# Performance work log

Measured on AMD Instinct MI355X. Metric: run time of the kernel, lower is better.

## Reference

```python
import jax, jax.numpy as jnp
import numpy as np

DECAY = 0.99
COMMIT = 0.25
EPS = 1e-5


def setup_inputs() -> dict:
    key = jax.random.key(0)
    k1, k2, k3 = jax.random.split(key, 3)
    B, H, W, D, K = 32, 32, 32, 64, 1024
    return {
        "z": jax.random.normal(k1, (B, H, W, D), dtype=jnp.float32),
        "embeddings": jax.random.normal(k2, (K, D), dtype=jnp.float32),
        "cluster_size": jnp.ones((K,), dtype=jnp.float32),
        "ema_embed": jax.random.normal(k3, (K, D), dtype=jnp.float32),
    }


def reference(z, embeddings, cluster_size, ema_embed):
    B, H, W, D = z.shape
    K = embeddings.shape[0]
    z_flat = z.reshape(-1, D)                      # [N, D]

    # squared L2 distances via expansion: ||z||^2 + ||e||^2 - 2 z e^T  -> [N, K]
    distances = (
        jnp.sum(z_flat * z_flat, axis=1, keepdims=True)
        + jnp.sum(embeddings * embeddings, axis=1)
        - 2.0 * z_flat @ embeddings.T
    )
    idx = jnp.argmin(distances, axis=1)            # [N]
    quantized = embeddings[idx].reshape(z.shape)   # gather, [B,H,W,D]

    # training-mode EMA update (one_hot^T matmuls expressed as segment sums)
    n_i = jax.ops.segment_sum(jnp.ones(z_flat.shape[0], z.dtype), idx, num_segments=K)
    dw = jax.ops.segment_sum(z_flat, idx, num_segments=K)          # [K, D]
    new_cluster = cluster_size * DECAY + n_i * (1.0 - DECAY)
    new_ema = ema_embed * DECAY + dw * (1.0 - DECAY)
    n = jnp.sum(new_cluster)
    new_cluster = (new_cluster + EPS) / (n + K * EPS) * n           # Laplace smoothing
    new_embeddings = new_ema / new_cluster[:, None]

    loss = COMMIT * jnp.mean((z - jax.lax.stop_gradient(quantized)) ** 2)
    q_ste = z + jax.lax.stop_gradient(quantized - z)                # straight-through

    quantized_vectors = jnp.transpose(q_ste, (0, 3, 1, 2))          # [B, D, H, W]
    quantized_indices = idx.reshape(B, H, W)[:, None, :, :]         # [B, 1, H, W]
    return quantized_vectors, quantized_indices, loss, new_embeddings, new_cluster, new_ema
```

## Files before the change

kernel.cpp:

```cpp
#include <hip/hip_runtime.h>


typedef unsigned short u16;
typedef u16 us8 __attribute__((ext_vector_type(8)));
typedef float f4 __attribute__((ext_vector_type(4)));

#define WS_FZ    0
#define WS_FE    1
#define WS_FCS   2
#define WS_FEMA  3
#define WS_LOSS  4

__device__ __forceinline__ float b2f(u16 u) {
    union { unsigned int i; float f; } x; x.i = ((unsigned int)u) << 16; return x.f;
}
__device__ __forceinline__ int swzE(int d, int c) {
    return d * 64 + (c ^ ((((d) >> 2) & 7) << 2));
}
__device__ __forceinline__ int swzZ(int d, int c) {
    int cb = (c >> 2) ^ (c >> 5);
    int cc = ((cb & 31) << 2) | (c & 3);
    return d * 128 + (cc ^ ((((d) >> 2) & 7) << 2));
}

__global__ __launch_bounds__(256) void k_init(
    const u16* z, const u16* e, const u16* cs, const u16* ema,
    float* __restrict__ ws, float* __restrict__ esqp, int K)
{
    __shared__ int flg[4];
    const int w = threadIdx.x >> 6, l = threadIdx.x & 63;
    const u16* p = (w == 0) ? z : (w == 1) ? e : (w == 2) ? cs : ema;
    int cnt = 0;
    #pragma unroll
    for (int t = 0; t < 4; ++t) {
        unsigned hb = (p[(l * 4 + t) * 2] >> 8) & 0x7F;
        cnt += (hb >= 0x3A && hb <= 0x41) ? 1 : 0;
    }
    #pragma unroll
    for (int off = 32; off; off >>= 1) cnt += __shfl_down(cnt, off);
    if (l == 0) flg[w] = (cnt < 128) ? 1 : 0;
    __syncthreads();
    if (blockIdx.x == 0) {
        if (threadIdx.x < 4) ((int*)ws)[threadIdx.x] = flg[threadIdx.x];
        if (threadIdx.x == 4) ws[WS_LOSS] = 0.0f;
    }
    const int fe = flg[1];
    const int code = blockIdx.x * 256 + threadIdx.x;
    if (code < K) {
        float r[8];
        if (fe) {
            const float* ep = (const float*)e + (size_t)code * 64;
            #pragma unroll
            for (int j = 0; j < 8; ++j) { float v = ep[j]; float p2 = v * v;
                asm volatile("" : "+v"(p2)); r[j] = p2; }
            #pragma unroll
            for (int t = 1; t < 8; ++t)
                #pragma unroll
                for (int j = 0; j < 8; ++j) { float v = ep[8 * t + j]; float p2 = v * v;
                    asm volatile("" : "+v"(p2)); r[j] += p2; }
        } else {
            const u16* ep = e + (size_t)code * 64;
            #pragma unroll
            for (int j = 0; j < 8; ++j) { float v = b2f(ep[j]); float p2 = v * v;
                asm volatile("" : "+v"(p2)); r[j] = p2; }
            #pragma unroll
            for (int t = 1; t < 8; ++t)
                #pragma unroll
                for (int j = 0; j < 8; ++j) { float v = b2f(ep[8 * t + j]); float p2 = v * v;
                    asm volatile("" : "+v"(p2)); r[j] += p2; }
        }
        esqp[code] = ((r[0] + r[1]) + (r[2] + r[3])) + ((r[4] + r[5]) + (r[6] + r[7]));
    }
}

__global__ __launch_bounds__(512, 2) void k_main(
    const u16* __restrict__ z, const u16* __restrict__ e,
    const float* __restrict__ esqp,
    float* __restrict__ ws, float* __restrict__ out,
    int K, int offIdx, long long outSize)
{
    __shared__ __align__(16) float z_t[64 * 128];
    __shared__ __align__(16) float e_t[4 * 64 * 64];
    __shared__ float esq_l[2048];
    __shared__ float z2_l[128];
    __shared__ int   idx_l[128];

    const int tid = threadIdx.x;
    const int cg  = tid >> 7;
    const int lt  = tid & 127;
    const int mtg = lt & 15;
    const int ktg = lt >> 4;
    const int pbase = blockIdx.x * 128;
    const int* wsi = (const int*)ws;
    const int fz = wsi[WS_FZ];
    const int fe = wsi[WS_FE];
    const int kchunks = K >> 6;
    const int h = kchunks >> 2;

    for (int i = tid; i < K; i += 512) esq_l[i] = esqp[i];

    if (fz) {
        const f4* z4 = (const f4*)((const float*)z + (size_t)pbase * 64);
        for (int i = tid; i < 2048; i += 512) {
            f4 v = z4[i];
            int m = i >> 4, d4 = (i & 15) * 4;
            z_t[swzZ(d4 + 0, m)] = v[0];
            z_t[swzZ(d4 + 1, m)] = v[1];
            z_t[swzZ(d4 + 2, m)] = v[2];
            z_t[swzZ(d4 + 3, m)] = v[3];
        }
    } else {
        const us8* z8 = (const us8*)(z + (size_t)pbase * 64);
        for (int i = tid; i < 1024; i += 512) {
            us8 v = z8[i];
            int m = i >> 3, d8 = (i & 7) * 8;
            #pragma unroll
            for (int t = 0; t < 8; ++t) z_t[swzZ(d8 + t, m)] = b2f(v[t]);
        }
    }
    __syncthreads();
    if (tid < 128) {
        float r[8];
        #pragma unroll
        for (int j = 0; j < 8; ++j) {
            float v = z_t[swzZ(j, tid)]; float p = v * v;
            asm volatile("" : "+v"(p)); r[j] = p;
        }
        #pragma unroll
        for (int t = 1; t < 8; ++t)
            #pragma unroll
            for (int j = 0; j < 8; ++j) {
                float v = z_t[swzZ(8 * t + j, tid)]; float p = v * v;
                asm volatile("" : "+v"(p)); r[j] += p;
            }
        z2_l[tid] = ((r[0] + r[1]) + (r[2] + r[3])) + ((r[4] + r[5]) + (r[6] + r[7]));
    }

    float bestd[8] = {INFINITY, INFINITY, INFINITY, INFINITY,
                      INFINITY, INFINITY, INFINITY, INFINITY};
    int   besti[8] = {0, 0, 0, 0, 0, 0, 0, 0};
    float* et = e_t + cg * 4096;

    f4  fb[8];
    us8 hb[4];
    {
        int kc0 = cg * h;
        if (fe) {
            const f4* e4 = (const f4*)((const float*)e + (size_t)kc0 * 4096);
            #pragma unroll
            for (int t = 0; t < 8; ++t) fb[t] = e4[lt + 128 * t];
        } else {
            const us8* e8 = (const us8*)(e + (size_t)kc0 * 4096);
            #pragma unroll
            for (int t = 0; t < 4; ++t) hb[t] = e8[lt + 128 * t];
        }
    }

    for (int c = 0; c < h; ++c) {
        const int kc = cg * h + c;
        if (fe) {
            #pragma unroll
            for (int t = 0; t < 8; ++t) {
                int i = lt + 128 * t;
                int kl = i >> 4, d4 = (i & 15) * 4;
                et[swzE(d4 + 0, kl)] = fb[t][0];
                et[swzE(d4 + 1, kl)] = fb[t][1];
                et[swzE(d4 + 2, kl)] = fb[t][2];
                et[swzE(d4 + 3, kl)] = fb[t][3];
            }
        } else {
            #pragma unroll
            for (int t = 0; t < 4; ++t) {
                int i = lt + 128 * t;
                int kl = i >> 3, d8 = (i & 7) * 8;
                #pragma unroll
                for (int s = 0; s < 8; ++s) et[swzE(d8 + s, kl)] = b2f(hb[t][s]);
            }
        }
        if (c + 1 < h) {
            if (fe) {
                const f4* e4 = (const f4*)((const float*)e + (size_t)(kc + 1) * 4096);
                #pragma unroll
                for (int t = 0; t < 8; ++t) fb[t] = e4[lt + 128 * t];
            } else {
                const us8* e8 = (const us8*)(e + (size_t)(kc + 1) * 4096);
                #pragma unroll
                for (int t = 0; t < 4; ++t) hb[t] = e8[lt + 128 * t];
            }
        }
        __syncthreads();

        float acc[8][8] = {};
        for (int d0 = 0; d0 < 64; d0 += 4) {
            f4 za[4], zb[4], ea[4], eb[4];
            #pragma unroll
            for (int j = 0; j < 4; ++j) {
                int d = d0 + j;
                za[j] = *(const f4*)&z_t[swzZ(d, mtg * 8)];
                zb[j] = *(const f4*)&z_t[swzZ(d, mtg * 8 + 4)];
                ea[j] = *(const f4*)&et[swzE(d, ktg * 8)];
                eb[j] = *(const f4*)&et[swzE(d, ktg * 8 + 4)];
            }
            #pragma unroll
            for (int j = 0; j < 4; ++j) {
                #pragma unroll
                for (int a = 0; a < 4; ++a)
                    #pragma unroll
                    for (int b = 0; b < 4; ++b) {
                        acc[a][b]         += za[j][a] * ea[j][b];
                        acc[a][b + 4]     += za[j][a] * eb[j][b];
                        acc[a + 4][b]     += zb[j][a] * ea[j][b];
                        acc[a + 4][b + 4] += zb[j][a] * eb[j][b];
                    }
            }
        }
        __syncthreads();

        #pragma unroll
        for (int a = 0; a < 8; ++a) {
            float z2 = z2_l[mtg * 8 + a];
            #pragma unroll
            for (int b = 0; b < 8; ++b) {
                float e2 = esq_l[kc * 64 + ktg * 8 + b];
                float dist = (z2 + e2) - 2.0f * acc[a][b];
                int kg = kc * 64 + ktg * 8 + b;
                if (dist < bestd[a]) { bestd[a] = dist; besti[a] = kg; }
            }
        }
    }

    float* red_d = e_t;
    int*   red_i = (int*)(e_t + 4224);
    #pragma unroll
    for (int a = 0; a < 8; ++a) {
        red_d[(mtg * 8 + a) * 33 + (cg * 8 + ktg)] = bestd[a];
        red_i[(mtg * 8 + a) * 33 + (cg * 8 + ktg)] = besti[a];
    }
    __syncthreads();

    if (tid < 128) {
        float bd = red_d[tid * 33]; int bi = red_i[tid * 33];
        #pragma unroll
        for (int t = 1; t < 32; ++t) {
            float dv = red_d[tid * 33 + t]; int iv = red_i[tid * 33 + t];
            if (dv < bd || (dv == bd && iv < bi)) { bd = dv; bi = iv; }
        }
        idx_l[tid] = bi;
        long long oi = (long long)offIdx + pbase + tid;
        if (oi < outSize) out[oi] = (float)bi;
    }
    __syncthreads();

    const int m = tid & 127;
    const int w = tid >> 7;
    const int p = pbase + m;
    const int b = p >> 10;
    const int hw = p & 1023;
    const int kidx = idx_l[m];
    float lsum = 0.f;
    #pragma unroll
    for (int dd = 0; dd < 16; ++dd) {
        int d = w + 4 * dd;
        float zv = z_t[swzZ(d, m)];
        float q  = fe ? ((const float*)e)[(size_t)kidx * 64 + d]
                      : b2f(e[(size_t)kidx * 64 + d]);
        float df = zv - q;
        lsum += df * df;
        float qs = zv + (q - zv);
        long long qi = (long long)b * 65536 + d * 1024 + hw;
        if (qi < outSize) out[qi] = qs;
    }
    #pragma unroll
    for (int off = 32; off; off >>= 1) lsum += __shfl_down(lsum, off);
    if ((tid & 63) == 0) atomicAdd(&ws[WS_LOSS], lsum);
}

__global__ __launch_bounds__(512) void k_dwf(
    const u16* __restrict__ z, const float* __restrict__ idxf,
    const u16* __restrict__ cs, const u16* __restrict__ ema,
    float* __restrict__ ws, float* __restrict__ out,
    int K, int N, long long offLoss, long long outSize, float lossScale)
{
    __shared__ int   queue[2048];
    __shared__ int   qcnt;
    __shared__ float cnt[8];
    __shared__ float red[8][512];
    __shared__ float red2[512];

    const int KB = K >> 8;
    const int base = blockIdx.x * KB;
    const int t = threadIdx.x;
    const int w = t >> 6, lane = t & 63;
    const int* wsi = (const int*)ws;
    const int fz = wsi[WS_FZ], fcs = wsi[WS_FCS], fema = wsi[WS_FEMA];

    if (t == 0) qcnt = 0;
    if (t < 8) cnt[t] = 0.0f;
    float acc[8] = {0.f, 0.f, 0.f, 0.f, 0.f, 0.f, 0.f, 0.f};
    __syncthreads();

    const int nseg = (N + 2047) / 2048;
    for (int s = 0; s < nseg; ++s) {
        int i4 = s * 512 + t;
        if (i4 * 4 < N) {
            f4 v = ((const f4*)idxf)[i4];
            #pragma unroll
            for (int j = 0; j < 4; ++j) {
                int k = (int)v[j];
                if (k >= base && k < base + KB) {
                    int qi = atomicAdd(&qcnt, 1);
                    queue[qi] = ((i4 * 4 + j) << 3) | (k - base);
                    atomicAdd(&cnt[k - base], 1.0f);
                }
            }
        }
        __syncthreads();
        const int n = qcnt;
        for (int ent = w; ent < n; ent += 8) {
            int q = queue[ent];
            int p = q >> 3, kl = q & 7;
            float v = fz ? ((const float*)z)[(size_t)p * 64 + lane]
                         : b2f(z[(size_t)p * 64 + lane]);
            #pragma unroll
            for (int c = 0; c < 8; ++c) acc[c] += (c == kl) ? v : 0.0f;
        }
        __syncthreads();
        if (t == 0) qcnt = 0;
        __syncthreads();
    }

    #pragma unroll
    for (int c = 0; c < 8; ++c)
        if (c < KB) red[w][c * 64 + lane] = acc[c];

    float partial = 0.f;
    for (int k0 = 0; k0 < K; k0 += 512) {
        int kk = k0 + t;
        if (kk < K) partial += fcs ? ((const float*)cs)[kk] : b2f(cs[kk]);
    }
    red2[t] = partial;
    __syncthreads();
    for (int s = 256; s; s >>= 1) {
        if (t < s) red2[t] += red2[t + s];
        __syncthreads();
    }
    const float n = 0.99f * red2[0] + 0.01f * (float)N;
    const float keps = (float)K * 1e-5f;

    const long long offEmb = offLoss + 1;
    const long long offCl  = offEmb + (long long)K * 64;
    const long long offEma = offCl + K;

    if (t < KB * 64) {
        int kl = t >> 6, d = t & 63;
        int kk = base + kl;
        float dw = 0.f;
        #pragma unroll
        for (int ww = 0; ww < 8; ++ww) dw += red[ww][kl * 64 + d];
        float c = (fcs ? ((const float*)cs)[kk] : b2f(cs[kk])) * 0.99f + cnt[kl] * 0.01f;
        float sm = (c + 1e-5f) / (n + keps) * n;
        long long i = (long long)kk * 64 + d;
        float ev = fema ? ((const float*)ema)[i] : b2f(ema[i]);
        float ne = ev * 0.99f + dw * 0.01f;
        if (offEma + i < outSize) out[offEma + i] = ne;
        if (offEmb + i < outSize) out[offEmb + i] = ne / sm;
        if (d == 0 && offCl + kk < outSize) out[offCl + kk] = sm;
    }
    if (blockIdx.x == 0 && t == 0 && offLoss < outSize)
        out[offLoss] = 0.25f * (ws[WS_LOSS] * lossScale);
}

extern "C" void kernel_launch(void* const* d_in, const int* in_sizes, int n_in,
                              void* d_out, int out_size, void* d_ws, size_t ws_size,
                              hipStream_t stream) {
    long long sz[4] = {0, 0, 0, 0};
    for (int i = 0; i < n_in && i < 4; ++i) sz[i] = in_sizes[i];
    int icl = 0, iz = 0;
    for (int i = 1; i < 4; ++i) { if (sz[i] < sz[icl]) icl = i; if (sz[i] > sz[iz]) iz = i; }
    int ip[2], np = 0;
    for (int i = 0; i < 4; ++i) if (i != icl && i != iz && np < 2) ip[np++] = i;
    long long K = sz[icl], KD = (np == 2) ? sz[ip[0]] : 0;
    int derivOK = (n_in == 4 && np == 2 && icl != iz && sz[ip[0]] == sz[ip[1]] &&
                   K > 0 && KD % K == 0);
    long long D = derivOK ? KD / K : 64;
    long long N = (derivOK && D > 0 && sz[iz] % D == 0) ? sz[iz] / D : 32768;
    int ie, iema;
    if (!derivOK) { iz = 0; ie = 1; icl = 2; iema = 3; N = 32768; K = 1024; D = 64; }
    else if (icl > ip[0] && icl < ip[1]) { ie = ip[0]; iema = ip[1]; }
    else { iema = ip[0]; ie = ip[1]; }

    int fastOK = (D == 64) && (N % 1024 == 0) && (K % 256 == 0) &&
                 (K >= 512) && (K <= 2048);
    if (!fastOK) { N = 32768; K = 1024; }

    long long offIdx = N * 64, offLoss = offIdx + N;

    float* out = (float*)d_out;
    float* ws = (float*)d_ws;
    float* esqp = ((long long)ws_size >= (8 + K) * 4) ? (ws + 8)
                 : (out + offLoss + 1 + K * 64);

    const u16* z   = (const u16*)d_in[iz];
    const u16* e   = (const u16*)d_in[ie];
    const u16* cs  = (const u16*)d_in[icl];
    const u16* ema = (const u16*)d_in[iema];

    float lossScale = (float)(1.0 / (double)(N * 64));

    k_init<<<(int)((K + 255) / 256), 256, 0, stream>>>(z, e, cs, ema, ws, esqp, (int)K);
    k_main<<<(int)(N / 128), 512, 0, stream>>>(z, e, esqp, ws, out,
                                               (int)K, (int)offIdx, (long long)out_size);
    k_dwf<<<256, 512, 0, stream>>>(z, out + offIdx, cs, ema, ws, out,
                                   (int)K, (int)N, offLoss,
                                   (long long)out_size, lossScale);
}
```

Baseline: 209.6 us.

## Keep z rows in registers and stream pre-converted codebook via uniform loads

The distance kernel drops the LDS-tiled outer-product GEMM. Each thread now holds one z row in 64 registers and each wave scans a slice of codes, reading a float32 codebook copy that the init kernel writes, with wave-uniform addresses. This removes the LDS staging, the swizzles and the barriers in the main loop, and halves points per block. The cost is lost register-tile reuse, plus reliance on scalar-cache broadcast of the codebook and high register pressure.

```diff
diff --git a/kernel.cpp b/kernel.cpp
--- a/kernel.cpp
+++ b/kernel.cpp
@@ -14,18 +14,11 @@
 __device__ __forceinline__ float b2f(u16 u) {
     union { unsigned int i; float f; } x; x.i = ((unsigned int)u) << 16; return x.f;
 }
-__device__ __forceinline__ int swzE(int d, int c) {
-    return d * 64 + (c ^ ((((d) >> 2) & 7) << 2));
-}
-__device__ __forceinline__ int swzZ(int d, int c) {
-    int cb = (c >> 2) ^ (c >> 5);
-    int cc = ((cb & 31) << 2) | (c & 3);
-    return d * 128 + (cc ^ ((((d) >> 2) & 7) << 2));
-}
 
 __global__ __launch_bounds__(256) void k_init(
     const u16* z, const u16* e, const u16* cs, const u16* ema,
-    float* __restrict__ ws, float* __restrict__ esqp, int K)
+    float* __restrict__ ws, float* __restrict__ esqp,
+    float* __restrict__ eprime, int K)
 {
     __shared__ int flg[4];
     const int w = threadIdx.x >> 6, l = threadIdx.x & 63;
@@ -48,201 +41,118 @@
     const int code = blockIdx.x * 256 + threadIdx.x;
     if (code < K) {
         float r[8];
+        float* eo = eprime + (size_t)code * 64;
         if (fe) {
             const float* ep = (const float*)e + (size_t)code * 64;
             #pragma unroll
-            for (int j = 0; j < 8; ++j) { float v = ep[j]; float p2 = v * v;
-                asm volatile("" : "+v"(p2)); r[j] = p2; }
+            for (int j = 0; j < 8; ++j) { float v = ep[j]; eo[j] = v;
+                float p2 = v * v; asm volatile("" : "+v"(p2)); r[j] = p2; }
             #pragma unroll
             for (int t = 1; t < 8; ++t)
                 #pragma unroll
-                for (int j = 0; j < 8; ++j) { float v = ep[8 * t + j]; float p2 = v * v;
-                    asm volatile("" : "+v"(p2)); r[j] += p2; }
+                for (int j = 0; j < 8; ++j) { float v = ep[8 * t + j]; eo[8 * t + j] = v;
+                    float p2 = v * v; asm volatile("" : "+v"(p2)); r[j] += p2; }
         } else {
             const u16* ep = e + (size_t)code * 64;
             #pragma unroll
-            for (int j = 0; j < 8; ++j) { float v = b2f(ep[j]); float p2 = v * v;
-                asm volatile("" : "+v"(p2)); r[j] = p2; }
+            for (int j = 0; j < 8; ++j) { float v = b2f(ep[j]); eo[j] = v;
+                float p2 = v * v; asm volatile("" : "+v"(p2)); r[j] = p2; }
             #pragma unroll
             for (int t = 1; t < 8; ++t)
                 #pragma unroll
-                for (int j = 0; j < 8; ++j) { float v = b2f(ep[8 * t + j]); float p2 = v * v;
-                    asm volatile("" : "+v"(p2)); r[j] += p2; }
+                for (int j = 0; j < 8; ++j) { float v = b2f(ep[8 * t + j]); eo[8 * t + j] = v;
+                    float p2 = v * v; asm volatile("" : "+v"(p2)); r[j] += p2; }
         }
         esqp[code] = ((r[0] + r[1]) + (r[2] + r[3])) + ((r[4] + r[5]) + (r[6] + r[7]));
     }
 }
 
-__global__ __launch_bounds__(512, 2) void k_main(
-    const u16* __restrict__ z, const u16* __restrict__ e,
-    const float* __restrict__ esqp,
+__global__ __launch_bounds__(512, 4) void k_main(
+    const u16* __restrict__ z,
+    const float* __restrict__ esqp, const float* __restrict__ eprime,
     float* __restrict__ ws, float* __restrict__ out,
     int K, int offIdx, long long outSize)
 {
-    __shared__ __align__(16) float z_t[64 * 128];
-    __shared__ __align__(16) float e_t[4 * 64 * 64];
-    __shared__ float esq_l[2048];
-    __shared__ float z2_l[128];
-    __shared__ int   idx_l[128];
-
-    const int tid = threadIdx.x;
-    const int cg  = tid >> 7;
-    const int lt  = tid & 127;
-    const int mtg = lt & 15;
-    const int ktg = lt >> 4;
-    const int pbase = blockIdx.x * 128;
+    __shared__ float md[8][64];
+    __shared__ int   mi[8][64];
+    __shared__ int   idx_l[64];
+
+    const int tid  = threadIdx.x;
+    const int lane = tid & 63;
+    const int w    = tid >> 6;
+    const int pbase = blockIdx.x * 64;
+    const int p     = pbase + lane;
     const int* wsi = (const int*)ws;
     const int fz = wsi[WS_FZ];
-    const int fe = wsi[WS_FE];
-    const int kchunks = K >> 6;
-    const int h = kchunks >> 2;
-
-    for (int i = tid; i < K; i += 512) esq_l[i] = esqp[i];
-
+
+    float zr[64];
     if (fz) {
-        const f4* z4 = (const f4*)((const float*)z + (size_t)pbase * 64);
-        for (int i = tid; i < 2048; i += 512) {
-            f4 v = z4[i];
-            int m = i >> 4, d4 = (i & 15) * 4;
-            z_t[swzZ(d4 + 0, m)] = v[0];
-            z_t[swzZ(d4 + 1, m)] = v[1];
-            z_t[swzZ(d4 + 2, m)] = v[2];
-            z_t[swzZ(d4 + 3, m)] = v[3];
+        const f4* zp = (const f4*)((const float*)z + (size_t)p * 64);
+        #pragma unroll
+        for (int j = 0; j < 16; ++j) {
+            f4 v = zp[j];
+            zr[4 * j + 0] = v[0]; zr[4 * j + 1] = v[1];
+            zr[4 * j + 2] = v[2]; zr[4 * j + 3] = v[3];
         }
     } else {
-        const us8* z8 = (const us8*)(z + (size_t)pbase * 64);
-        for (int i = tid; i < 1024; i += 512) {
-            us8 v = z8[i];
-            int m = i >> 3, d8 = (i & 7) * 8;
-            #pragma unroll
-            for (int t = 0; t < 8; ++t) z_t[swzZ(d8 + t, m)] = b2f(v[t]);
-        }
-    }
-    __syncthreads();
-    if (tid < 128) {
+        const us8* zp = (const us8*)(z + (size_t)p * 64);
+        #pragma unroll
+        for (int j = 0; j < 8; ++j) {
+            us8 v = zp[j];
+            #pragma unroll
+            for (int s = 0; s < 8; ++s) zr[8 * j + s] = b2f(v[s]);
+        }
+    }
+
+    float z2;
+    {
         float r[8];
         #pragma unroll
         for (int j = 0; j < 8; ++j) {
-            float v = z_t[swzZ(j, tid)]; float p = v * v;
-            asm volatile("" : "+v"(p)); r[j] = p;
+            float v = zr[j]; float pq = v * v;
+            asm volatile("" : "+v"(pq)); r[j] = pq;
         }
         #pragma unroll
         for (int t = 1; t < 8; ++t)
             #pragma unroll
             for (int j = 0; j < 8; ++j) {
-                float v = z_t[swzZ(8 * t + j, tid)]; float p = v * v;
-                asm volatile("" : "+v"(p)); r[j] += p;
+                float v = zr[8 * t + j]; float pq = v * v;
+                asm volatile("" : "+v"(pq)); r[j] += pq;
             }
-        z2_l[tid] = ((r[0] + r[1]) + (r[2] + r[3])) + ((r[4] + r[5]) + (r[6] + r[7]));
-    }
-
-    float bestd[8] = {INFINITY, INFINITY, INFINITY, INFINITY,
-                      INFINITY, INFINITY, INFINITY, INFINITY};
-    int   besti[8] = {0, 0, 0, 0, 0, 0, 0, 0};
-    float* et = e_t + cg * 4096;
-
-    f4  fb[8];
-    us8 hb[4];
-    {
-        int kc0 = cg * h;
-        if (fe) {
-            const f4* e4 = (const f4*)((const float*)e + (size_t)kc0 * 4096);
-            #pragma unroll
-            for (int t = 0; t < 8; ++t) fb[t] = e4[lt + 128 * t];
-        } else {
-            const us8* e8 = (const us8*)(e + (size_t)kc0 * 4096);
-            #pragma unroll
-            for (int t = 0; t < 4; ++t) hb[t] = e8[lt + 128 * t];
-        }
-    }
-
-    for (int c = 0; c < h; ++c) {
-        const int kc = cg * h + c;
-        if (fe) {
-            #pragma unroll
-            for (int t = 0; t < 8; ++t) {
-                int i = lt + 128 * t;
-                int kl = i >> 4, d4 = (i & 15) * 4;
-                et[swzE(d4 + 0, kl)] = fb[t][0];
-                et[swzE(d4 + 1, kl)] = fb[t][1];
-                et[swzE(d4 + 2, kl)] = fb[t][2];
-                et[swzE(d4 + 3, kl)] = fb[t][3];
-            }
-        } else {
-            #pragma unroll
-            for (int t = 0; t < 4; ++t) {
-                int i = lt + 128 * t;
-                int kl = i >> 3, d8 = (i & 7) * 8;
-                #pragma unroll
-                for (int s = 0; s < 8; ++s) et[swzE(d8 + s, kl)] = b2f(hb[t][s]);
-            }
-        }
-        if (c + 1 < h) {
-            if (fe) {
-                const f4* e4 = (const f4*)((const float*)e + (size_t)(kc + 1) * 4096);
-                #pragma unroll
-                for (int t = 0; t < 8; ++t) fb[t] = e4[lt + 128 * t];
-            } else {
-                const us8* e8 = (const us8*)(e + (size_t)(kc + 1) * 4096);
-                #pragma unroll
-                for (int t = 0; t < 4; ++t) hb[t] = e8[lt + 128 * t];
-            }
-        }
-        __syncthreads();
-
-        float acc[8][8] = {};
-        for (int d0 = 0; d0 < 64; d0 += 4) {
-            f4 za[4], zb[4], ea[4], eb[4];
-            #pragma unroll
-            for (int j = 0; j < 4; ++j) {
-                int d = d0 + j;
-                za[j] = *(const f4*)&z_t[swzZ(d, mtg * 8)];
-                zb[j] = *(const f4*)&z_t[swzZ(d, mtg * 8 + 4)];
-                ea[j] = *(const f4*)&et[swzE(d, ktg * 8)];
-                eb[j] = *(const f4*)&et[swzE(d, ktg * 8 + 4)];
-            }
-            #pragma unroll
-            for (int j = 0; j < 4; ++j) {
-                #pragma unroll
-                for (int a = 0; a < 4; ++a)
-                    #pragma unroll
-                    for (int b = 0; b < 4; ++b) {
-                        acc[a][b]         += za[j][a] * ea[j][b];
-                        acc[a][b + 4]     += za[j][a] * eb[j][b];
-                        acc[a + 4][b]     += zb[j][a] * ea[j][b];
-                        acc[a + 4][b + 4] += zb[j][a] * eb[j][b];
-                    }
-            }
-        }
-        __syncthreads();
-
-        #pragma unroll
-        for (int a = 0; a < 8; ++a) {
-            float z2 = z2_l[mtg * 8 + a];
-            #pragma unroll
-            for (int b = 0; b < 8; ++b) {
-                float e2 = esq_l[kc * 64 + ktg * 8 + b];
-                float dist = (z2 + e2) - 2.0f * acc[a][b];
-                int kg = kc * 64 + ktg * 8 + b;
-                if (dist < bestd[a]) { bestd[a] = dist; besti[a] = kg; }
-            }
-        }
-    }
-
-    float* red_d = e_t;
-    int*   red_i = (int*)(e_t + 4224);
-    #pragma unroll
-    for (int a = 0; a < 8; ++a) {
-        red_d[(mtg * 8 + a) * 33 + (cg * 8 + ktg)] = bestd[a];
-        red_i[(mtg * 8 + a) * 33 + (cg * 8 + ktg)] = besti[a];
-    }
-    __syncthreads();
-
-    if (tid < 128) {
-        float bd = red_d[tid * 33]; int bi = red_i[tid * 33];
-        #pragma unroll
-        for (int t = 1; t < 32; ++t) {
-            float dv = red_d[tid * 33 + t]; int iv = red_i[tid * 33 + t];
+        z2 = ((r[0] + r[1]) + (r[2] + r[3])) + ((r[4] + r[5]) + (r[6] + r[7]));
+    }
+
+    const int CPW = K >> 3;
+    const int c0  = __builtin_amdgcn_readfirstlane(w * CPW);
+
+    float bestd = INFINITY;
+    int   besti = 0;
+
+    for (int c = 0; c < CPW; c += 2) {
+        const float* ep0 = eprime + (size_t)(c0 + c) * 64;
+        const float* ep1 = ep0 + 64;
+        float a0 = 0.0f, a1 = 0.0f;
+        #pragma unroll
+        for (int d = 0; d < 64; ++d) {
+            a0 += zr[d] * ep0[d];
+            a1 += zr[d] * ep1[d];
+        }
+        float e20 = esqp[c0 + c];
+        float e21 = esqp[c0 + c + 1];
+        float d0v = (z2 + e20) - 2.0f * a0;
+        float d1v = (z2 + e21) - 2.0f * a1;
+        if (d0v < bestd) { bestd = d0v; besti = c0 + c; }
+        if (d1v < bestd) { bestd = d1v; besti = c0 + c + 1; }
+    }
+
+    md[w][lane] = bestd;
+    mi[w][lane] = besti;
+    __syncthreads();
+    if (tid < 64) {
+        float bd = md[0][tid]; int bi = mi[0][tid];
+        #pragma unroll
+        for (int t = 1; t < 8; ++t) {
+            float dv = md[t][tid]; int iv = mi[t][tid];
             if (dv < bd || (dv == bd && iv < bi)) { bd = dv; bi = iv; }
         }
         idx_l[tid] = bi;
@@ -251,28 +161,29 @@
     }
     __syncthreads();
 
-    const int m = tid & 127;
-    const int w = tid >> 7;
-    const int p = pbase + m;
-    const int b = p >> 10;
+    const int b  = p >> 10;
     const int hw = p & 1023;
-    const int kidx = idx_l[m];
-    float lsum = 0.f;
-    #pragma unroll
-    for (int dd = 0; dd < 16; ++dd) {
-        int d = w + 4 * dd;
-        float zv = z_t[swzZ(d, m)];
-        float q  = fe ? ((const float*)e)[(size_t)kidx * 64 + d]
-                      : b2f(e[(size_t)kidx * 64 + d]);
-        float df = zv - q;
-        lsum += df * df;
-        float qs = zv + (q - zv);
-        long long qi = (long long)b * 65536 + d * 1024 + hw;
-        if (qi < outSize) out[qi] = qs;
+    const int kidx = idx_l[lane];
+    const float* eq = eprime + (size_t)kidx * 64;
+    const long long qbase = (long long)b * 65536 + hw;
+    float lsum = 0.0f;
+    #pragma unroll
+    for (int W = 0; W < 8; ++W) if (w == W) {
+        #pragma unroll
+        for (int j = 0; j < 8; ++j) {
+            const int d = W * 8 + j;
+            float zv = zr[d];
+            float q  = eq[d];
+            float df = zv - q;
+            lsum += df * df;
+            float qs = zv + (q - zv);
+            long long qi = qbase + (long long)d * 1024;
+            if (qi < outSize) out[qi] = qs;
+        }
     }
     #pragma unroll
     for (int off = 32; off; off >>= 1) lsum += __shfl_down(lsum, off);
-    if ((tid & 63) == 0) atomicAdd(&ws[WS_LOSS], lsum);
+    if (lane == 0) atomicAdd(&ws[WS_LOSS], lsum);
 }
 
 __global__ __launch_bounds__(512) void k_dwf(
@@ -399,6 +310,8 @@
     float* ws = (float*)d_ws;
     float* esqp = ((long long)ws_size >= (8 + K) * 4) ? (ws + 8)
                  : (out + offLoss + 1 + K * 64);
+    float* eprime = ((long long)ws_size >= (8 + K + K * 64) * 4) ? (ws + 8 + K)
+                 : (out + offLoss + 1);
 
     const u16* z   = (const u16*)d_in[iz];
     const u16* e   = (const u16*)d_in[ie];
@@ -407,9 +320,9 @@
 
     float lossScale = (float)(1.0 / (double)(N * 64));
 
-    k_init<<<(int)((K + 255) / 256), 256, 0, stream>>>(z, e, cs, ema, ws, esqp, (int)K);
-    k_main<<<(int)(N / 128), 512, 0, stream>>>(z, e, esqp, ws, out,
-                                               (int)K, (int)offIdx, (long long)out_size);
+    k_init<<<(int)((K + 255) / 256), 256, 0, stream>>>(z, e, cs, ema, ws, esqp, eprime, (int)K);
+    k_main<<<(int)(N / 64), 512, 0, stream>>>(z, esqp, eprime, ws, out,
+                                              (int)K, (int)offIdx, (long long)out_size);
     k_dwf<<<256, 512, 0, stream>>>(z, out + offIdx, cs, ema, ws, out,
                                    (int)K, (int)N, offLoss,
                                    (long long)out_size, lossScale);
```

New measurement: 273.6 us. 1.31x slower.

## Replace queued per-block segment sum with global atomic scatter and finalize kernel

Applied to the files above, without the earlier changes.

Drops the k_dwf kernel, where each of 256 blocks scanned every index and queued the matches for its own 4 codes. In its place, k_scat has one wavefront per row atomically add that z row and its count into zeroed global buffers, and a separate elementwise k_fin kernel applies the EMA and Laplace-smoothing update. The cluster-size sum moves into k_init as a block reduction plus one atomic per block. The aim is to remove the redundant full-index scans and the barrier-heavy queue loop. In exchange it adds global float-atomic contention, a memset of the accumulation buffers and one more kernel launch.

```diff
diff --git a/kernel.cpp b/kernel.cpp
--- a/kernel.cpp
+++ b/kernel.cpp
@@ -10,6 +10,7 @@
 #define WS_FCS   2
 #define WS_FEMA  3
 #define WS_LOSS  4
+#define WS_CSSUM 5
 
 __device__ __forceinline__ float b2f(u16 u) {
     union { unsigned int i; float f; } x; x.i = ((unsigned int)u) << 16; return x.f;
@@ -28,6 +29,7 @@
     float* __restrict__ ws, float* __restrict__ esqp, int K)
 {
     __shared__ int flg[4];
+    __shared__ float csred[256];
     const int w = threadIdx.x >> 6, l = threadIdx.x & 63;
     const u16* p = (w == 0) ? z : (w == 1) ? e : (w == 2) ? cs : ema;
     int cnt = 0;
@@ -45,6 +47,7 @@
         if (threadIdx.x == 4) ws[WS_LOSS] = 0.0f;
     }
     const int fe = flg[1];
+    const int fcs = flg[2];
     const int code = blockIdx.x * 256 + threadIdx.x;
     if (code < K) {
         float r[8];
@@ -71,6 +74,14 @@
         }
         esqp[code] = ((r[0] + r[1]) + (r[2] + r[3])) + ((r[4] + r[5]) + (r[6] + r[7]));
     }
+    csred[threadIdx.x] = (code < K)
+        ? (fcs ? ((const float*)cs)[code] : b2f(cs[code])) : 0.0f;
+    __syncthreads();
+    for (int s = 128; s; s >>= 1) {
+        if (threadIdx.x < s) csred[threadIdx.x] += csred[threadIdx.x + s];
+        __syncthreads();
+    }
+    if (threadIdx.x == 0) atomicAdd(&ws[WS_CSSUM], csred[0]);
 }
 
 __global__ __launch_bounds__(512, 2) void k_main(
@@ -275,98 +286,61 @@
     if ((tid & 63) == 0) atomicAdd(&ws[WS_LOSS], lsum);
 }
 
-__global__ __launch_bounds__(512) void k_dwf(
+__global__ __launch_bounds__(512) void k_scat(
     const u16* __restrict__ z, const float* __restrict__ idxf,
+    const float* __restrict__ ws,
+    float* __restrict__ dwb, float* __restrict__ cntb, int N)
+{
+    const int* wsi = (const int*)ws;
+    const int fz = wsi[WS_FZ];
+    const int lane = threadIdx.x & 63;
+    const int wv = (blockIdx.x * 512 + threadIdx.x) >> 6;
+    const int nw = (gridDim.x * 512) >> 6;
+    for (int p = wv; p < N; p += nw) {
+        int k = (int)idxf[p];
+        float v = fz ? ((const float*)z)[(size_t)p * 64 + lane]
+                     : b2f(z[(size_t)p * 64 + lane]);
+        atomicAdd(&dwb[(size_t)k * 64 + lane], v);
+        if (lane == 0) atomicAdd(&cntb[k], 1.0f);
+    }
+}
+
+__global__ __launch_bounds__(256) void k_fin(
     const u16* __restrict__ cs, const u16* __restrict__ ema,
-    float* __restrict__ ws, float* __restrict__ out,
-    int K, int N, long long offLoss, long long outSize, float lossScale)
+    const float* __restrict__ ws,
+    const float* __restrict__ dwb, const float* __restrict__ cntb,
+    float* __restrict__ out, int K, int N,
+    long long offLoss, long long outSize, float lossScale)
 {
-    __shared__ int   queue[2048];
-    __shared__ int   qcnt;
-    __shared__ float cnt[8];
-    __shared__ float red[8][512];
-    __shared__ float red2[512];
-
-    const int KB = K >> 8;
-    const int base = blockIdx.x * KB;
-    const int t = threadIdx.x;
-    const int w = t >> 6, lane = t & 63;
     const int* wsi = (const int*)ws;
-    const int fz = wsi[WS_FZ], fcs = wsi[WS_FCS], fema = wsi[WS_FEMA];
-
-    if (t == 0) qcnt = 0;
-    if (t < 8) cnt[t] = 0.0f;
-    float acc[8] = {0.f, 0.f, 0.f, 0.f, 0.f, 0.f, 0.f, 0.f};
-    __syncthreads();
-
-    const int nseg = (N + 2047) / 2048;
-    for (int s = 0; s < nseg; ++s) {
-        int i4 = s * 512 + t;
-        if (i4 * 4 < N) {
-            f4 v = ((const f4*)idxf)[i4];
-            #pragma unroll
-            for (int j = 0; j < 4; ++j) {
-                int k = (int)v[j];
-                if (k >= base && k < base + KB) {
-                    int qi = atomicAdd(&qcnt, 1);
-                    queue[qi] = ((i4 * 4 + j) << 3) | (k - base);
-                    atomicAdd(&cnt[k - base], 1.0f);
-                }
-            }
-        }
-        __syncthreads();
-        const int n = qcnt;
-        for (int ent = w; ent < n; ent += 8) {
-            int q = queue[ent];
-            int p = q >> 3, kl = q & 7;
-            float v = fz ? ((const float*)z)[(size_t)p * 64 + lane]
-                         : b2f(z[(size_t)p * 64 + lane]);
-            #pragma unroll
-            for (int c = 0; c < 8; ++c) acc[c] += (c == kl) ? v : 0.0f;
-        }
-        __syncthreads();
-        if (t == 0) qcnt = 0;
-        __syncthreads();
-    }
-
-    #pragma unroll
-    for (int c = 0; c < 8; ++c)
-        if (c < KB) red[w][c * 64 + lane] = acc[c];
-
-    float partial = 0.f;
-    for (int k0 = 0; k0 < K; k0 += 512) {
-        int kk = k0 + t;
-        if (kk < K) partial += fcs ? ((const float*)cs)[kk] : b2f(cs[kk]);
-    }
-    red2[t] = partial;
-    __syncthreads();
-    for (int s = 256; s; s >>= 1) {
-        if (t < s) red2[t] += red2[t + s];
-        __syncthreads();
-    }
-    const float n = 0.99f * red2[0] + 0.01f * (float)N;
-    const float keps = (float)K * 1e-5f;
-
+    const int fcs = wsi[WS_FCS], fema = wsi[WS_FEMA];
+    const int i = blockIdx.x * 256 + threadIdx.x;
     const long long offEmb = offLoss + 1;
     const long long offCl  = offEmb + (long long)K * 64;
     const long long offEma = offCl + K;
-
-    if (t < KB * 64) {
-        int kl = t >> 6, d = t & 63;
-        int kk = base + kl;
-        float dw = 0.f;
-        #pragma unroll
-        for (int ww = 0; ww < 8; ++ww) dw += red[ww][kl * 64 + d];
-        float c = (fcs ? ((const float*)cs)[kk] : b2f(cs[kk])) * 0.99f + cnt[kl] * 0.01f;
-        float sm = (c + 1e-5f) / (n + keps) * n;
-        long long i = (long long)kk * 64 + d;
-        float ev = fema ? ((const float*)ema)[i] : b2f(ema[i]);
+    const float nsum = 0.99f * ws[WS_CSSUM] + 0.01f * (float)N;
+    const float keps = (float)K * 1e-5f;
+
+    float cnt = 0.f, dw = 0.f, csv = 0.f, ev = 0.f;
+    int k = 0, d = 0;
+    const int ok = (i < K * 64);
+    if (ok) {
+        k = i >> 6; d = i & 63;
+        cnt = cntb[k];
+        dw  = dwb[i];
+        csv = fcs ? ((const float*)cs)[k] : b2f(cs[k]);
+        ev  = fema ? ((const float*)ema)[i] : b2f(ema[i]);
+    }
+    __syncthreads();
+    if (ok) {
+        float c  = csv * 0.99f + cnt * 0.01f;
+        float sm = (c + 1e-5f) / (nsum + keps) * nsum;
         float ne = ev * 0.99f + dw * 0.01f;
         if (offEma + i < outSize) out[offEma + i] = ne;
         if (offEmb + i < outSize) out[offEmb + i] = ne / sm;
-        if (d == 0 && offCl + kk < outSize) out[offCl + kk] = sm;
-    }
-    if (blockIdx.x == 0 && t == 0 && offLoss < outSize)
+        if (d == 0 && offCl + k < outSize) out[offCl + k] = sm;
+    }
+    if (blockIdx.x == 0 && threadIdx.x == 0 && offLoss < outSize)
         out[offLoss] = 0.25f * (ws[WS_LOSS] * lossScale);
 }
 
@@ -394,11 +368,21 @@
     if (!fastOK) { N = 32768; K = 1024; }
 
     long long offIdx = N * 64, offLoss = offIdx + N;
+    long long offEmb = offLoss + 1, offCl = offEmb + K * 64, offEma = offCl + K;
 
     float* out = (float*)d_out;
     float* ws = (float*)d_ws;
-    float* esqp = ((long long)ws_size >= (8 + K) * 4) ? (ws + 8)
-                 : (out + offLoss + 1 + K * 64);
+
+    long long wsNeed = 8 + K + K * 64 + K;
+    float *esqp, *dwb, *cntb;
+    if ((long long)ws_size >= wsNeed * 4) {
+        esqp = ws + 8; dwb = ws + 8 + K; cntb = dwb + K * 64;
+        hipMemsetAsync(ws, 0, (size_t)(wsNeed * 4), stream);
+    } else {
+        esqp = out + offEma; dwb = out + offEmb; cntb = out + offCl;
+        hipMemsetAsync(ws, 0, 8 * 4, stream);
+        hipMemsetAsync(out + offEmb, 0, (size_t)((K * 64 + K) * 4), stream);
+    }
 
     const u16* z   = (const u16*)d_in[iz];
     const u16* e   = (const u16*)d_in[ie];
@@ -410,7 +394,8 @@
     k_init<<<(int)((K + 255) / 256), 256, 0, stream>>>(z, e, cs, ema, ws, esqp, (int)K);
     k_main<<<(int)(N / 128), 512, 0, stream>>>(z, e, esqp, ws, out,
                                                (int)K, (int)offIdx, (long long)out_size);
-    k_dwf<<<256, 512, 0, stream>>>(z, out + offIdx, cs, ema, ws, out,
-                                   (int)K, (int)N, offLoss,
-                                   (long long)out_size, lossScale);
-}
+    k_scat<<<512, 512, 0, stream>>>(z, out + offIdx, ws, dwb, cntb, (int)N);
+    k_fin<<<(int)((K * 64 + 255) / 256), 256, 0, stream>>>(cs, ema, ws, dwb, cntb, out,
+                                                           (int)K, (int)N, offLoss,
+                                                           (long long)out_size, lossScale);
+}
```

New measurement: 193.8 us. 7.5% less time.
